# Performance work log

Measured on AMD Instinct MI355X. Metric: run time of the kernel, lower is better.

The kernel has to match this reference:

```python
import jax, jax.numpy as jnp
import numpy as np

B, T, I, H = 64, 188, 512, 1024
R = H  # recurrent_size == hidden_size (required for the cell math to be consistent)


def setup_inputs() -> dict:
    key = jax.random.key(0)
    ks = jax.random.split(key, 6)
    stdv = 1.0 / np.sqrt(H)
    u = lambda k, shape: jax.random.uniform(k, shape, jnp.float32, -stdv, stdv)
    return {
        "x": jax.random.normal(ks[0], (B, T, I), jnp.float32),
        "h0": jnp.zeros((B, R), jnp.float32),
        "c0": jnp.zeros((B, H), jnp.float32),
        "weight_ih": u(ks[1], (4 * H, I)),
        "weight_hh": u(ks[2], (4 * H, R)),
        "weight_rec": u(ks[3], (2 * R, H)),
        "bias": u(ks[4], (4 * H,)),
        "lengths": jax.random.randint(ks[5], (B,), 1, T + 1),
    }


def reference(x, h0, c0, weight_ih, weight_hh, weight_rec, bias, lengths):
    # length_matrix[j][t] == 1 iff t < lengths[j]; state is zeroed where 0
    mask = (jnp.arange(T)[:, None] < lengths[None, :]).astype(x.dtype)[:, :, None]  # [T,B,1]
    # precompute input projections for all timesteps: [T, B, 4H]
    pre_x = jnp.einsum('bti,gi->tbg', x, weight_ih) + bias

    def step(carry, inp):
        h, c = carry
        px, m = inp
        pre = px + h @ weight_hh.T           # [B, 4H]
        pre_c = c @ weight_rec.T             # [B, 2R] (peephole)
        i = jax.nn.sigmoid(pre[:, :H] + pre_c[:, :H])
        f = jax.nn.sigmoid(pre[:, H:2 * H] + pre_c[:, H:2 * H])
        g = jnp.tanh(pre[:, 2 * H:3 * H])
        c_new = f * c + i * g
        o = jax.nn.sigmoid(pre[:, 3 * H:] + c_new)
        h_new = o * jnp.tanh(c_new)
        h_new = h_new * m  # zero finished sequences (index_fill_ with 0)
        c_new = c_new * m
        return (h_new, c_new), (h_new, c_new)

    (_, _), (hs, cs) = jax.lax.scan(step, (h0, c0), (pre_x, mask))
    # stack over time then transpose(0,1) as in torch -> [B, T, H]
    return jnp.swapaxes(hs, 0, 1), jnp.swapaxes(cs, 0, 1)
```

## Files before the change

kernel.cpp:

```cpp
#include <hip/hip_runtime.h>


#define T_N 188

#define WS_PX     0UL
#define WS_XB     98566144UL
#define WS_WIHB   110886912UL
#define WS_WCOMB  115081216UL
#define WS_HST    127664128UL
#define WS_CST    127926272UL
#define WS_FLAGS  128188416UL
#define WS_WRECLO 128192512UL
#define WS_CSTLO  132386816UL

typedef __attribute__((ext_vector_type(8))) short short8;
typedef __attribute__((ext_vector_type(4))) float f4;

__device__ __forceinline__ float b2f(unsigned short u) {
    union { unsigned int i; float f; } v; v.i = ((unsigned int)u) << 16; return v.f;
}
__device__ __forceinline__ unsigned short f2b(float f) {
    unsigned int u = __float_as_uint(f);
    return (unsigned short)((u + 0x7FFFu + ((u >> 16) & 1u)) >> 16);
}
__device__ __forceinline__ float sigf(float x) { return 1.0f / (1.0f + __expf(-x)); }
__device__ __forceinline__ float tanh_(float x) {
    float e = __expf(2.0f * x); return 1.0f - 2.0f / (e + 1.0f);
}
#define MFMA(a, b, c) __builtin_amdgcn_mfma_f32_16x16x32_bf16((a), (b), (c), 0, 0, 0)

#define LD16(dst, addr) \
    asm volatile("global_load_dwordx4 %0, %1, off sc0 sc1" : "=&v"(dst) : "v"(addr))

#define BALLAST(bal)                                                       \
    _Pragma("unroll")                                                      \
    for (int u_ = 0; u_ < 16; ++u_) bal = __builtin_fmaf(bal, 1.0000001f, 1e-7f)

__device__ __forceinline__ f4 px_init(const unsigned short* px, int t, int gate, int jg, int brow) {
    unsigned long long pv =
        *(const unsigned long long*)(px + ((long)(t * 4 + gate) * 1024 + jg) * 64 + brow);
    f4 r;
    r[0] = b2f((unsigned short)pv);
    r[1] = b2f((unsigned short)(pv >> 16));
    r[2] = b2f((unsigned short)(pv >> 32));
    r[3] = b2f((unsigned short)(pv >> 48));
    return r;
}

__global__ void k_prep(const float* __restrict__ x, const float* __restrict__ h0,
                       const float* __restrict__ c0, const float* __restrict__ wih,
                       const float* __restrict__ whh, const float* __restrict__ wrec,
                       unsigned short* __restrict__ xb, unsigned short* __restrict__ wihb,
                       unsigned short* __restrict__ wcomb, unsigned short* __restrict__ hst,
                       unsigned short* __restrict__ cst, unsigned short* __restrict__ wreclo,
                       unsigned short* __restrict__ cstlo, int* __restrict__ flags) {
    const long NX4 = 1540096, NWIH4 = 524288, NWHH4 = 1048576, NWREC4 = 524288, NH4 = 16384;
    const long total = NX4 + NWIH4 + NWHH4 + NWREC4 + NH4 + NH4;
    long gtid = (long)blockIdx.x * blockDim.x + threadIdx.x;
    for (long i = gtid; i < total; i += (long)gridDim.x * blockDim.x) {
        const float* src; unsigned short* dst; unsigned short* lo_dst = nullptr; long off = i;
        if (off < NX4)                   { src = x;    dst = xb; }
        else if ((off -= NX4) < NWIH4)   { src = wih;  dst = wihb; }
        else if ((off -= NWIH4) < NWHH4) { src = whh;  dst = wcomb; }
        else if ((off -= NWHH4) < NWREC4){ src = wrec; dst = wcomb + 4194304; lo_dst = wreclo; }
        else if ((off -= NWREC4) < NH4)  { src = h0;   dst = hst + 65536; }
        else { off -= NH4;                 src = c0;   dst = cst + 65536; lo_dst = cstlo + 65536; }
        float4 v = ((const float4*)src)[off];
        unsigned short hx = f2b(v.x), hy = f2b(v.y), hz = f2b(v.z), hw = f2b(v.w);
        unsigned long long o = (unsigned long long)hx
            | ((unsigned long long)hy << 16)
            | ((unsigned long long)hz << 32)
            | ((unsigned long long)hw << 48);
        *(unsigned long long*)(dst + off * 4) = o;
        if (lo_dst) {
            unsigned long long l = (unsigned long long)f2b(v.x - b2f(hx))
                | ((unsigned long long)f2b(v.y - b2f(hy)) << 16)
                | ((unsigned long long)f2b(v.z - b2f(hz)) << 32)
                | ((unsigned long long)f2b(v.w - b2f(hw)) << 48);
            *(unsigned long long*)(lo_dst + off * 4) = l;
        }
    }
    if (gtid < 1024) flags[gtid] = 0;
}

__global__ void __launch_bounds__(256) k_px(const unsigned short* __restrict__ xb,
                                            const unsigned short* __restrict__ wihb,
                                            const float* __restrict__ bias,
                                            unsigned short* __restrict__ px) {
    const int t = blockIdx.y;
    const int wv = threadIdx.x >> 6, lane = threadIdx.x & 63;
    const int col = lane & 15, quad = lane >> 4;
    const int n = blockIdx.x * 64 + wv * 16 + col;
    const float bn = bias[n];
    f4 acc[4];
#pragma unroll
    for (int mt = 0; mt < 4; ++mt) { acc[mt][0] = bn; acc[mt][1] = bn; acc[mt][2] = bn; acc[mt][3] = bn; }
    const unsigned short* bp = wihb + n * 512 + quad * 8;
#pragma unroll 4
    for (int kk = 0; kk < 16; ++kk) {
        short8 bf = *(const short8*)(bp + kk * 32);
#pragma unroll
        for (int mt = 0; mt < 4; ++mt) {
            const unsigned short* ap = xb + ((mt * 16 + col) * 188 + t) * 512 + kk * 32 + quad * 8;
            short8 af = *(const short8*)ap;
            acc[mt] = MFMA(af, bf, acc[mt]);
        }
    }
    const long pb = ((long)(t * 4 + (n >> 10)) * 1024 + (n & 1023)) * 64;
#pragma unroll
    for (int mt = 0; mt < 4; ++mt) {
        unsigned long long o = (unsigned long long)f2b(acc[mt][0])
            | ((unsigned long long)f2b(acc[mt][1]) << 16)
            | ((unsigned long long)f2b(acc[mt][2]) << 32)
            | ((unsigned long long)f2b(acc[mt][3]) << 48);
        *(unsigned long long*)(px + pb + mt * 16 + quad * 4) = o;
    }
}

__global__ void __launch_bounds__(256, 1) k_scan(
    const unsigned short* __restrict__ wcomb, const unsigned short* __restrict__ wreclo,
    const float* __restrict__ c0, const int* __restrict__ lengths,
    const unsigned short* __restrict__ px, unsigned short* __restrict__ hst,
    unsigned short* __restrict__ cst, unsigned short* __restrict__ cstlo,
    int* __restrict__ flags, float* __restrict__ out) {
    const int cu = blockIdx.x;
    const int g = cu >> 6, cig = cu & 63;
    const int jbase = cig * 16, b0 = g * 16;
    const int tid = threadIdx.x, wv = tid >> 6, lane = tid & 63;
    const int kh = wv >> 1, ts = wv & 1;
    const int kbase = kh * 512;
    const int col = lane & 15, quad = lane >> 4;

    __shared__ float pre[2][2][6][16][16];
    __shared__ float c_loc[16][16];
    __shared__ int go_word;

    short8 wf[4][16];
#pragma unroll
    for (int tile = 0; tile < 4; ++tile) {
        const unsigned short* src;
        if (ts == 0) {
            src = wcomb + (long)(tile * 1024 + jbase + col) * 1024 + kbase + quad * 8;
        } else if (tile < 2) {
            src = wcomb + (long)((4 + tile) * 1024 + jbase + col) * 1024 + kbase + quad * 8;
        } else {
            src = wreclo + (long)((tile - 2) * 1024 + jbase + col) * 1024 + kbase + quad * 8;
        }
#pragma unroll
        for (int kk = 0; kk < 16; ++kk) wf[tile][kk] = *(const short8*)(src + kk * 32);
    }
    {
        int b = tid >> 4, j = tid & 15;
        c_loc[b][j] = c0[(b0 + b) * 1024 + jbase + j];
    }
    if (tid == 0) go_word = 0;
    const int my_len = lengths[b0 + (tid >> 4)];
    float bal = (float)lane + 1.0f;
    __syncthreads();

    float* out_h = out;
    float* out_c = out + 12320768;

    for (int t = 0; t < T_N; ++t) {
        const int sl_r = (t + 1) & 1, sl_w = t & 1, ps = t & 1;

        f4 pxv[4];
        if (ts == 0 && kh == 0) {
#pragma unroll
            for (int tile = 0; tile < 4; ++tile)
                pxv[tile] = px_init(px, t, tile, jbase + col, b0 + quad * 4);
        }

        if (t > 0) {
            if (wv == 0) {
                const int* fp = flags + g * 64 + lane;
                for (;;) {
                    int a = __hip_atomic_load(fp, __ATOMIC_RELAXED, __HIP_MEMORY_SCOPE_AGENT);
                    if (__all(a >= t)) break;
                    BALLAST(bal);
                }
                if (lane == 0)
                    __hip_atomic_store(&go_word, t, __ATOMIC_RELAXED, __HIP_MEMORY_SCOPE_WORKGROUP);
            } else {
                for (;;) {
                    int gw = __hip_atomic_load(&go_word, __ATOMIC_RELAXED, __HIP_MEMORY_SCOPE_WORKGROUP);
                    if (gw >= t) break;
                    BALLAST(bal);
                }
            }
            asm volatile("" ::: "memory");
        }

        const int sbase = sl_r * 65536 + (b0 + col) * 1024 + kbase + quad * 8;

        if (ts == 0) {
            const unsigned short* hp = hst + sbase;
            short8 hbuf[16];
#pragma unroll
            for (int kk = 0; kk < 16; ++kk) LD16(hbuf[kk], hp + kk * 32);
            f4 acc[4];
#pragma unroll
            for (int tile = 0; tile < 4; ++tile) {
                if (kh == 0) acc[tile] = pxv[tile];
                else { acc[tile][0] = 0.f; acc[tile][1] = 0.f; acc[tile][2] = 0.f; acc[tile][3] = 0.f; }
            }
            asm volatile("s_waitcnt vmcnt(0)" ::: "memory");
            __builtin_amdgcn_sched_barrier(0);
#pragma unroll
            for (int kk = 0; kk < 16; ++kk) {
                acc[0] = MFMA(hbuf[kk], wf[0][kk], acc[0]);
                acc[1] = MFMA(hbuf[kk], wf[1][kk], acc[1]);
                acc[2] = MFMA(hbuf[kk], wf[2][kk], acc[2]);
                acc[3] = MFMA(hbuf[kk], wf[3][kk], acc[3]);
            }
#pragma unroll
            for (int tile = 0; tile < 4; ++tile)
#pragma unroll
                for (int r = 0; r < 4; ++r) pre[ps][kh][tile][quad * 4 + r][col] = acc[tile][r];
        } else {
            const unsigned short* cph = cst + sbase;
            const unsigned short* cpl = cstlo + sbase;
            short8 chb[16], clb[16];
#pragma unroll
            for (int kk = 0; kk < 16; ++kk) LD16(chb[kk], cph + kk * 32);
#pragma unroll
            for (int kk = 0; kk < 16; ++kk) LD16(clb[kk], cpl + kk * 32);
            f4 a0 = {0.f, 0.f, 0.f, 0.f}, a1 = a0, a2 = a0, a3 = a0, a4 = a0, a5 = a0;
            asm volatile("s_waitcnt vmcnt(0)" ::: "memory");
            __builtin_amdgcn_sched_barrier(0);
#pragma unroll
            for (int kk = 0; kk < 16; ++kk) {
                a0 = MFMA(chb[kk], wf[0][kk], a0);
                a1 = MFMA(chb[kk], wf[1][kk], a1);
                a2 = MFMA(chb[kk], wf[2][kk], a2);
                a3 = MFMA(chb[kk], wf[3][kk], a3);
                a4 = MFMA(clb[kk], wf[0][kk], a4);
                a5 = MFMA(clb[kk], wf[1][kk], a5);
            }
#pragma unroll
            for (int r = 0; r < 4; ++r) {
                pre[ps][kh][4][quad * 4 + r][col] = a0[r] + a2[r] + a4[r];
                pre[ps][kh][5][quad * 4 + r][col] = a1[r] + a3[r] + a5[r];
            }
        }
        __syncthreads();

        float hn, cn; long ob;
        {
            const int b = tid >> 4, j = tid & 15;
            float pi = pre[ps][0][0][b][j] + pre[ps][1][0][b][j] + pre[ps][0][4][b][j] + pre[ps][1][4][b][j];
            float pf = pre[ps][0][1][b][j] + pre[ps][1][1][b][j] + pre[ps][0][5][b][j] + pre[ps][1][5][b][j];
            float pg = pre[ps][0][2][b][j] + pre[ps][1][2][b][j];
            float po = pre[ps][0][3][b][j] + pre[ps][1][3][b][j];
            const float cprev = c_loc[b][j];
            const float iv = sigf(pi), fv = sigf(pf), gv = tanh_(pg);
            cn = fv * cprev + iv * gv;
            float ov = sigf(po + cn);
            hn = ov * tanh_(cn);
            if (t >= my_len) { hn = 0.f; cn = 0.f; }
            c_loc[b][j] = cn;
            ob = (long)(b0 + b) * 192512 + (long)t * 1024 + jbase + j;
            const int sidx = sl_w * 65536 + (b0 + b) * 1024 + jbase + j;
            unsigned short hb  = f2b(hn);
            unsigned short chb2 = f2b(cn);
            unsigned short clb2 = f2b(cn - b2f(chb2));
            __hip_atomic_store(&hst[sidx],  hb,   __ATOMIC_RELAXED, __HIP_MEMORY_SCOPE_AGENT);
            __hip_atomic_store(&cst[sidx],  chb2, __ATOMIC_RELAXED, __HIP_MEMORY_SCOPE_AGENT);
            __hip_atomic_store(&cstlo[sidx], clb2, __ATOMIC_RELAXED, __HIP_MEMORY_SCOPE_AGENT);
        }
        asm volatile("s_waitcnt vmcnt(0)" ::: "memory");
        __syncthreads();
        if (tid == 0)
            __hip_atomic_store(&flags[cu], t + 1, __ATOMIC_RELAXED, __HIP_MEMORY_SCOPE_AGENT);
        out_h[ob] = hn;
        out_c[ob] = cn;
    }
    asm volatile("" :: "v"(bal));
}

extern "C" void kernel_launch(void* const* d_in, const int* in_sizes, int n_in,
                              void* d_out, int out_size, void* d_ws, size_t ws_size,
                              hipStream_t stream) {
    const float* x    = (const float*)d_in[0];
    const float* h0   = (const float*)d_in[1];
    const float* c0   = (const float*)d_in[2];
    const float* wih  = (const float*)d_in[3];
    const float* whh  = (const float*)d_in[4];
    const float* wrec = (const float*)d_in[5];
    const float* bias = (const float*)d_in[6];
    const int* lengths = (const int*)d_in[7];

    char* ws = (char*)d_ws;
    unsigned short* px     = (unsigned short*)(ws + WS_PX);
    unsigned short* xb     = (unsigned short*)(ws + WS_XB);
    unsigned short* wihb   = (unsigned short*)(ws + WS_WIHB);
    unsigned short* wcomb  = (unsigned short*)(ws + WS_WCOMB);
    unsigned short* hst    = (unsigned short*)(ws + WS_HST);
    unsigned short* cst    = (unsigned short*)(ws + WS_CST);
    unsigned short* wreclo = (unsigned short*)(ws + WS_WRECLO);
    unsigned short* cstlo  = (unsigned short*)(ws + WS_CSTLO);
    int* flags             = (int*)(ws + WS_FLAGS);
    float* out = (float*)d_out;

    hipLaunchKernelGGL(k_prep, dim3(2048), dim3(256), 0, stream,
                       x, h0, c0, wih, whh, wrec, xb, wihb, wcomb, hst, cst, wreclo, cstlo, flags);
    hipLaunchKernelGGL(k_px, dim3(64, 188), dim3(256), 0, stream, xb, wihb, bias, px);
    hipLaunchKernelGGL(k_scan, dim3(256), dim3(256), 0, stream,
                       wcomb, wreclo, c0, lengths, px, hst, cst, cstlo, flags, out);
}
```

Baseline: 1.658 ms.

## Split recurrent matmul K-dimension across all four waves and use per-wave flags

Each of the four waves now handles a quarter of the K dimension for every gate and peephole tile, replacing the earlier split of two K-halves by two tile sets. This balances MFMA work evenly across waves and shortens each wave's dependent chain. The second __syncthreads after the state stores is removed: each wave publishes its own flag, and the poller reads four flags per CU with one dwordx4 load. The spin-wait ballast is also widened to four independent FMA chains. The cost is more shared-memory partials to reduce and more flag traffic. The flag array now needs four times as many slots, and it is unclear whether the host zeroes that larger range.

```diff
diff --git a/kernel.cpp b/kernel.cpp
--- a/kernel.cpp
+++ b/kernel.cpp
@@ -15,6 +15,7 @@
 
 typedef __attribute__((ext_vector_type(8))) short short8;
 typedef __attribute__((ext_vector_type(4))) float f4;
+typedef __attribute__((ext_vector_type(4))) int int4v;
 
 __device__ __forceinline__ float b2f(unsigned short u) {
     union { unsigned int i; float f; } v; v.i = ((unsigned int)u) << 16; return v.f;
@@ -32,9 +33,14 @@
 #define LD16(dst, addr) \
     asm volatile("global_load_dwordx4 %0, %1, off sc0 sc1" : "=&v"(dst) : "v"(addr))
 
-#define BALLAST(bal)                                                       \
+#define BAL64()                                                            \
     _Pragma("unroll")                                                      \
-    for (int u_ = 0; u_ < 16; ++u_) bal = __builtin_fmaf(bal, 1.0000001f, 1e-7f)
+    for (int u_ = 0; u_ < 16; ++u_) {                                      \
+        bl0 = __builtin_fmaf(bl0, 1.0000001f, 1e-7f);                      \
+        bl1 = __builtin_fmaf(bl1, 1.0000001f, 2e-7f);                      \
+        bl2 = __builtin_fmaf(bl2, 1.0000001f, 3e-7f);                      \
+        bl3 = __builtin_fmaf(bl3, 1.0000001f, 4e-7f);                      \
+    }
 
 __device__ __forceinline__ f4 px_init(const unsigned short* px, int t, int gate, int jg, int brow) {
     unsigned long long pv =
@@ -127,35 +133,37 @@
     const int g = cu >> 6, cig = cu & 63;
     const int jbase = cig * 16, b0 = g * 16;
     const int tid = threadIdx.x, wv = tid >> 6, lane = tid & 63;
-    const int kh = wv >> 1, ts = wv & 1;
-    const int kbase = kh * 512;
+    const int kbase = wv * 256;
     const int col = lane & 15, quad = lane >> 4;
-
-    __shared__ float pre[2][2][6][16][16];
+    const int b_ = tid >> 4, j_ = tid & 15;
+
+    __shared__ float pre[2][4][6][16][16];
     __shared__ float c_loc[16][16];
     __shared__ int go_word;
 
-    short8 wf[4][16];
-#pragma unroll
-    for (int tile = 0; tile < 4; ++tile) {
-        const unsigned short* src;
-        if (ts == 0) {
-            src = wcomb + (long)(tile * 1024 + jbase + col) * 1024 + kbase + quad * 8;
-        } else if (tile < 2) {
-            src = wcomb + (long)((4 + tile) * 1024 + jbase + col) * 1024 + kbase + quad * 8;
-        } else {
-            src = wreclo + (long)((tile - 2) * 1024 + jbase + col) * 1024 + kbase + quad * 8;
-        }
-#pragma unroll
-        for (int kk = 0; kk < 16; ++kk) wf[tile][kk] = *(const short8*)(src + kk * 32);
-    }
-    {
-        int b = tid >> 4, j = tid & 15;
-        c_loc[b][j] = c0[(b0 + b) * 1024 + jbase + j];
-    }
+    short8 wg[4][8];
+    short8 wh[2][8];
+    short8 wl[2][8];
+#pragma unroll
+    for (int gate = 0; gate < 4; ++gate) {
+        const unsigned short* src = wcomb + (long)(gate * 1024 + jbase + col) * 1024 + kbase + quad * 8;
+#pragma unroll
+        for (int kk = 0; kk < 8; ++kk) wg[gate][kk] = *(const short8*)(src + kk * 32);
+    }
+#pragma unroll
+    for (int tl = 0; tl < 2; ++tl) {
+        const unsigned short* sh = wcomb + (long)((4 + tl) * 1024 + jbase + col) * 1024 + kbase + quad * 8;
+        const unsigned short* sl = wreclo + (long)(tl * 1024 + jbase + col) * 1024 + kbase + quad * 8;
+#pragma unroll
+        for (int kk = 0; kk < 8; ++kk) {
+            wh[tl][kk] = *(const short8*)(sh + kk * 32);
+            wl[tl][kk] = *(const short8*)(sl + kk * 32);
+        }
+    }
+    c_loc[b_][j_] = c0[(b0 + b_) * 1024 + jbase + j_];
     if (tid == 0) go_word = 0;
-    const int my_len = lengths[b0 + (tid >> 4)];
-    float bal = (float)lane + 1.0f;
+    const int my_len = lengths[b0 + b_];
+    float bl0 = (float)lane + 1.0f, bl1 = bl0 + 0.5f, bl2 = bl0 + 0.25f, bl3 = bl0 + 0.125f;
     __syncthreads();
 
     float* out_h = out;
@@ -165,7 +173,7 @@
         const int sl_r = (t + 1) & 1, sl_w = t & 1, ps = t & 1;
 
         f4 pxv[4];
-        if (ts == 0 && kh == 0) {
+        if (wv == 0) {
 #pragma unroll
             for (int tile = 0; tile < 4; ++tile)
                 pxv[tile] = px_init(px, t, tile, jbase + col, b0 + quad * 4);
@@ -173,11 +181,16 @@
 
         if (t > 0) {
             if (wv == 0) {
-                const int* fp = flags + g * 64 + lane;
+                const int* fp = flags + (g * 64 + lane) * 4;
                 for (;;) {
-                    int a = __hip_atomic_load(fp, __ATOMIC_RELAXED, __HIP_MEMORY_SCOPE_AGENT);
-                    if (__all(a >= t)) break;
-                    BALLAST(bal);
+                    int4v fvv;
+                    asm volatile("global_load_dwordx4 %0, %1, off sc0 sc1" : "=&v"(fvv) : "v"(fp));
+                    asm volatile("s_waitcnt vmcnt(0)" ::: "memory");
+                    int m0 = fvv[0] < fvv[1] ? fvv[0] : fvv[1];
+                    int m1 = fvv[2] < fvv[3] ? fvv[2] : fvv[3];
+                    int m = m0 < m1 ? m0 : m1;
+                    if (__all(m >= t)) break;
+                    BAL64();
                 }
                 if (lane == 0)
                     __hip_atomic_store(&go_word, t, __ATOMIC_RELAXED, __HIP_MEMORY_SCOPE_WORKGROUP);
@@ -185,7 +198,7 @@
                 for (;;) {
                     int gw = __hip_atomic_load(&go_word, __ATOMIC_RELAXED, __HIP_MEMORY_SCOPE_WORKGROUP);
                     if (gw >= t) break;
-                    BALLAST(bal);
+                    BAL64();
                 }
             }
             asm volatile("" ::: "memory");
@@ -193,89 +206,82 @@
 
         const int sbase = sl_r * 65536 + (b0 + col) * 1024 + kbase + quad * 8;
 
-        if (ts == 0) {
-            const unsigned short* hp = hst + sbase;
-            short8 hbuf[16];
-#pragma unroll
-            for (int kk = 0; kk < 16; ++kk) LD16(hbuf[kk], hp + kk * 32);
-            f4 acc[4];
-#pragma unroll
-            for (int tile = 0; tile < 4; ++tile) {
-                if (kh == 0) acc[tile] = pxv[tile];
-                else { acc[tile][0] = 0.f; acc[tile][1] = 0.f; acc[tile][2] = 0.f; acc[tile][3] = 0.f; }
+        short8 hb[8], cb[8], lb[8];
+#pragma unroll
+        for (int kk = 0; kk < 8; ++kk) LD16(hb[kk], hst + sbase + kk * 32);
+#pragma unroll
+        for (int kk = 0; kk < 8; ++kk) LD16(cb[kk], cst + sbase + kk * 32);
+#pragma unroll
+        for (int kk = 0; kk < 8; ++kk) LD16(lb[kk], cstlo + sbase + kk * 32);
+
+        f4 ag0, ag1, ag2, ag3;
+        if (wv == 0) { ag0 = pxv[0]; ag1 = pxv[1]; ag2 = pxv[2]; ag3 = pxv[3]; }
+        else {
+            ag0[0] = 0.f; ag0[1] = 0.f; ag0[2] = 0.f; ag0[3] = 0.f;
+            ag1 = ag0; ag2 = ag0; ag3 = ag0;
+        }
+        f4 ap0 = {0.f, 0.f, 0.f, 0.f}, ap1 = ap0, ap2 = ap0, ap3 = ap0, ap4 = ap0, ap5 = ap0;
+
+        asm volatile("s_waitcnt vmcnt(0)" ::: "memory");
+        __builtin_amdgcn_sched_barrier(0);
+#pragma unroll
+        for (int kk = 0; kk < 8; ++kk) {
+            ag0 = MFMA(hb[kk], wg[0][kk], ag0);
+            ag1 = MFMA(hb[kk], wg[1][kk], ag1);
+            ag2 = MFMA(hb[kk], wg[2][kk], ag2);
+            ag3 = MFMA(hb[kk], wg[3][kk], ag3);
+            ap0 = MFMA(cb[kk], wh[0][kk], ap0);
+            ap1 = MFMA(cb[kk], wh[1][kk], ap1);
+            ap2 = MFMA(cb[kk], wl[0][kk], ap2);
+            ap3 = MFMA(cb[kk], wl[1][kk], ap3);
+            ap4 = MFMA(lb[kk], wh[0][kk], ap4);
+            ap5 = MFMA(lb[kk], wh[1][kk], ap5);
+        }
+#pragma unroll
+        for (int r = 0; r < 4; ++r) {
+            pre[ps][wv][0][quad * 4 + r][col] = ag0[r];
+            pre[ps][wv][1][quad * 4 + r][col] = ag1[r];
+            pre[ps][wv][2][quad * 4 + r][col] = ag2[r];
+            pre[ps][wv][3][quad * 4 + r][col] = ag3[r];
+            pre[ps][wv][4][quad * 4 + r][col] = ap0[r] + ap2[r] + ap4[r];
+            pre[ps][wv][5][quad * 4 + r][col] = ap1[r] + ap3[r] + ap5[r];
+        }
+        __syncthreads();
+
+        float hn, cn;
+        {
+            float pi = 0.f, pf = 0.f, pg = 0.f, po = 0.f;
+#pragma unroll
+            for (int q = 0; q < 4; ++q) {
+                pi += pre[ps][q][0][b_][j_] + pre[ps][q][4][b_][j_];
+                pf += pre[ps][q][1][b_][j_] + pre[ps][q][5][b_][j_];
+                pg += pre[ps][q][2][b_][j_];
+                po += pre[ps][q][3][b_][j_];
             }
-            asm volatile("s_waitcnt vmcnt(0)" ::: "memory");
-            __builtin_amdgcn_sched_barrier(0);
-#pragma unroll
-            for (int kk = 0; kk < 16; ++kk) {
-                acc[0] = MFMA(hbuf[kk], wf[0][kk], acc[0]);
-                acc[1] = MFMA(hbuf[kk], wf[1][kk], acc[1]);
-                acc[2] = MFMA(hbuf[kk], wf[2][kk], acc[2]);
-                acc[3] = MFMA(hbuf[kk], wf[3][kk], acc[3]);
-            }
-#pragma unroll
-            for (int tile = 0; tile < 4; ++tile)
-#pragma unroll
-                for (int r = 0; r < 4; ++r) pre[ps][kh][tile][quad * 4 + r][col] = acc[tile][r];
-        } else {
-            const unsigned short* cph = cst + sbase;
-            const unsigned short* cpl = cstlo + sbase;
-            short8 chb[16], clb[16];
-#pragma unroll
-            for (int kk = 0; kk < 16; ++kk) LD16(chb[kk], cph + kk * 32);
-#pragma unroll
-            for (int kk = 0; kk < 16; ++kk) LD16(clb[kk], cpl + kk * 32);
-            f4 a0 = {0.f, 0.f, 0.f, 0.f}, a1 = a0, a2 = a0, a3 = a0, a4 = a0, a5 = a0;
-            asm volatile("s_waitcnt vmcnt(0)" ::: "memory");
-            __builtin_amdgcn_sched_barrier(0);
-#pragma unroll
-            for (int kk = 0; kk < 16; ++kk) {
-                a0 = MFMA(chb[kk], wf[0][kk], a0);
-                a1 = MFMA(chb[kk], wf[1][kk], a1);
-                a2 = MFMA(chb[kk], wf[2][kk], a2);
-                a3 = MFMA(chb[kk], wf[3][kk], a3);
-                a4 = MFMA(clb[kk], wf[0][kk], a4);
-                a5 = MFMA(clb[kk], wf[1][kk], a5);
-            }
-#pragma unroll
-            for (int r = 0; r < 4; ++r) {
-                pre[ps][kh][4][quad * 4 + r][col] = a0[r] + a2[r] + a4[r];
-                pre[ps][kh][5][quad * 4 + r][col] = a1[r] + a3[r] + a5[r];
-            }
-        }
-        __syncthreads();
-
-        float hn, cn; long ob;
-        {
-            const int b = tid >> 4, j = tid & 15;
-            float pi = pre[ps][0][0][b][j] + pre[ps][1][0][b][j] + pre[ps][0][4][b][j] + pre[ps][1][4][b][j];
-            float pf = pre[ps][0][1][b][j] + pre[ps][1][1][b][j] + pre[ps][0][5][b][j] + pre[ps][1][5][b][j];
-            float pg = pre[ps][0][2][b][j] + pre[ps][1][2][b][j];
-            float po = pre[ps][0][3][b][j] + pre[ps][1][3][b][j];
-            const float cprev = c_loc[b][j];
+            const float cprev = c_loc[b_][j_];
             const float iv = sigf(pi), fv = sigf(pf), gv = tanh_(pg);
             cn = fv * cprev + iv * gv;
             float ov = sigf(po + cn);
             hn = ov * tanh_(cn);
             if (t >= my_len) { hn = 0.f; cn = 0.f; }
-            c_loc[b][j] = cn;
-            ob = (long)(b0 + b) * 192512 + (long)t * 1024 + jbase + j;
-            const int sidx = sl_w * 65536 + (b0 + b) * 1024 + jbase + j;
-            unsigned short hb  = f2b(hn);
-            unsigned short chb2 = f2b(cn);
-            unsigned short clb2 = f2b(cn - b2f(chb2));
-            __hip_atomic_store(&hst[sidx],  hb,   __ATOMIC_RELAXED, __HIP_MEMORY_SCOPE_AGENT);
-            __hip_atomic_store(&cst[sidx],  chb2, __ATOMIC_RELAXED, __HIP_MEMORY_SCOPE_AGENT);
-            __hip_atomic_store(&cstlo[sidx], clb2, __ATOMIC_RELAXED, __HIP_MEMORY_SCOPE_AGENT);
+            c_loc[b_][j_] = cn;
+            const int sidx = sl_w * 65536 + (b0 + b_) * 1024 + jbase + j_;
+            unsigned short hbw  = f2b(hn);
+            unsigned short chw  = f2b(cn);
+            unsigned short clw  = f2b(cn - b2f(chw));
+            __hip_atomic_store(&hst[sidx],   hbw, __ATOMIC_RELAXED, __HIP_MEMORY_SCOPE_AGENT);
+            __hip_atomic_store(&cst[sidx],   chw, __ATOMIC_RELAXED, __HIP_MEMORY_SCOPE_AGENT);
+            __hip_atomic_store(&cstlo[sidx], clw, __ATOMIC_RELAXED, __HIP_MEMORY_SCOPE_AGENT);
         }
         asm volatile("s_waitcnt vmcnt(0)" ::: "memory");
-        __syncthreads();
-        if (tid == 0)
-            __hip_atomic_store(&flags[cu], t + 1, __ATOMIC_RELAXED, __HIP_MEMORY_SCOPE_AGENT);
+        if (lane == 0)
+            __hip_atomic_store(&flags[cu * 4 + wv], t + 1,
+                               __ATOMIC_RELAXED, __HIP_MEMORY_SCOPE_AGENT);
+        const long ob = (long)(b0 + b_) * 192512 + (long)t * 1024 + jbase + j_;
         out_h[ob] = hn;
         out_c[ob] = cn;
     }
-    asm volatile("" :: "v"(bal));
+    asm volatile("" :: "v"(bl0), "v"(bl1), "v"(bl2), "v"(bl3));
 }
 
 extern "C" void kernel_launch(void* const* d_in, const int* in_sizes, int n_in,
```

Result: slower. 1.691 ms (+2.0%).

## Convert recurrent weights to bf16 in scan kernel; widen input-projection tiles

Applied to the files above, without the earlier changes.

The scan kernel now loads the fp32 whh and wrec matrices directly and converts them to bf16 (with a hi/lo split for wrec) into registers at startup. This drops the prep kernel's conversion pass and its workspace round trip. Separately, the input-projection GEMM kernel gives each wave a 4x4 grid of MFMA tiles instead of 4x1, reusing A and B fragments more and launching a quarter as many blocks. The cost is twice as much global read in scan's prologue, more conversion work there, and higher register pressure in k_px.

```diff
diff --git a/kernel.cpp b/kernel.cpp
--- a/kernel.cpp
+++ b/kernel.cpp
@@ -49,22 +49,18 @@
 
 __global__ void k_prep(const float* __restrict__ x, const float* __restrict__ h0,
                        const float* __restrict__ c0, const float* __restrict__ wih,
-                       const float* __restrict__ whh, const float* __restrict__ wrec,
                        unsigned short* __restrict__ xb, unsigned short* __restrict__ wihb,
-                       unsigned short* __restrict__ wcomb, unsigned short* __restrict__ hst,
-                       unsigned short* __restrict__ cst, unsigned short* __restrict__ wreclo,
+                       unsigned short* __restrict__ hst, unsigned short* __restrict__ cst,
                        unsigned short* __restrict__ cstlo, int* __restrict__ flags) {
-    const long NX4 = 1540096, NWIH4 = 524288, NWHH4 = 1048576, NWREC4 = 524288, NH4 = 16384;
-    const long total = NX4 + NWIH4 + NWHH4 + NWREC4 + NH4 + NH4;
+    const long NX4 = 1540096, NWIH4 = 524288, NH4 = 16384;
+    const long total = NX4 + NWIH4 + NH4 + NH4;
     long gtid = (long)blockIdx.x * blockDim.x + threadIdx.x;
     for (long i = gtid; i < total; i += (long)gridDim.x * blockDim.x) {
         const float* src; unsigned short* dst; unsigned short* lo_dst = nullptr; long off = i;
-        if (off < NX4)                   { src = x;    dst = xb; }
-        else if ((off -= NX4) < NWIH4)   { src = wih;  dst = wihb; }
-        else if ((off -= NWIH4) < NWHH4) { src = whh;  dst = wcomb; }
-        else if ((off -= NWHH4) < NWREC4){ src = wrec; dst = wcomb + 4194304; lo_dst = wreclo; }
-        else if ((off -= NWREC4) < NH4)  { src = h0;   dst = hst + 65536; }
-        else { off -= NH4;                 src = c0;   dst = cst + 65536; lo_dst = cstlo + 65536; }
+        if (off < NX4)                  { src = x;   dst = xb; }
+        else if ((off -= NX4) < NWIH4)  { src = wih; dst = wihb; }
+        else if ((off -= NWIH4) < NH4)  { src = h0;  dst = hst + 65536; }
+        else { off -= NH4;                src = c0;  dst = cst + 65536; lo_dst = cstlo + 65536; }
         float4 v = ((const float4*)src)[off];
         unsigned short hx = f2b(v.x), hy = f2b(v.y), hz = f2b(v.z), hw = f2b(v.w);
         unsigned long long o = (unsigned long long)hx
@@ -90,35 +86,48 @@
     const int t = blockIdx.y;
     const int wv = threadIdx.x >> 6, lane = threadIdx.x & 63;
     const int col = lane & 15, quad = lane >> 4;
-    const int n = blockIdx.x * 64 + wv * 16 + col;
-    const float bn = bias[n];
-    f4 acc[4];
-#pragma unroll
-    for (int mt = 0; mt < 4; ++mt) { acc[mt][0] = bn; acc[mt][1] = bn; acc[mt][2] = bn; acc[mt][3] = bn; }
-    const unsigned short* bp = wihb + n * 512 + quad * 8;
+    const int nb = blockIdx.x * 256 + wv * 64;
+    f4 acc[4][4];
+#pragma unroll
+    for (int nt = 0; nt < 4; ++nt) {
+        const float bn = bias[nb + nt * 16 + col];
+#pragma unroll
+        for (int mt = 0; mt < 4; ++mt) {
+            acc[mt][nt][0] = bn; acc[mt][nt][1] = bn; acc[mt][nt][2] = bn; acc[mt][nt][3] = bn;
+        }
+    }
 #pragma unroll 4
     for (int kk = 0; kk < 16; ++kk) {
-        short8 bf = *(const short8*)(bp + kk * 32);
+        short8 bf[4], af[4];
+#pragma unroll
+        for (int nt = 0; nt < 4; ++nt)
+            bf[nt] = *(const short8*)(wihb + (nb + nt * 16 + col) * 512 + kk * 32 + quad * 8);
+#pragma unroll
+        for (int mt = 0; mt < 4; ++mt)
+            af[mt] = *(const short8*)(xb + ((mt * 16 + col) * 188 + t) * 512 + kk * 32 + quad * 8);
+#pragma unroll
+        for (int mt = 0; mt < 4; ++mt)
+#pragma unroll
+            for (int nt = 0; nt < 4; ++nt)
+                acc[mt][nt] = MFMA(af[mt], bf[nt], acc[mt][nt]);
+    }
+#pragma unroll
+    for (int nt = 0; nt < 4; ++nt) {
+        const int n = nb + nt * 16 + col;
+        const long pb = ((long)(t * 4 + (n >> 10)) * 1024 + (n & 1023)) * 64;
 #pragma unroll
         for (int mt = 0; mt < 4; ++mt) {
-            const unsigned short* ap = xb + ((mt * 16 + col) * 188 + t) * 512 + kk * 32 + quad * 8;
-            short8 af = *(const short8*)ap;
-            acc[mt] = MFMA(af, bf, acc[mt]);
-        }
-    }
-    const long pb = ((long)(t * 4 + (n >> 10)) * 1024 + (n & 1023)) * 64;
-#pragma unroll
-    for (int mt = 0; mt < 4; ++mt) {
-        unsigned long long o = (unsigned long long)f2b(acc[mt][0])
-            | ((unsigned long long)f2b(acc[mt][1]) << 16)
-            | ((unsigned long long)f2b(acc[mt][2]) << 32)
-            | ((unsigned long long)f2b(acc[mt][3]) << 48);
-        *(unsigned long long*)(px + pb + mt * 16 + quad * 4) = o;
+            unsigned long long o = (unsigned long long)f2b(acc[mt][nt][0])
+                | ((unsigned long long)f2b(acc[mt][nt][1]) << 16)
+                | ((unsigned long long)f2b(acc[mt][nt][2]) << 32)
+                | ((unsigned long long)f2b(acc[mt][nt][3]) << 48);
+            *(unsigned long long*)(px + pb + mt * 16 + quad * 4) = o;
+        }
     }
 }
 
 __global__ void __launch_bounds__(256, 1) k_scan(
-    const unsigned short* __restrict__ wcomb, const unsigned short* __restrict__ wreclo,
+    const float* __restrict__ whh, const float* __restrict__ wrec,
     const float* __restrict__ c0, const int* __restrict__ lengths,
     const unsigned short* __restrict__ px, unsigned short* __restrict__ hst,
     unsigned short* __restrict__ cst, unsigned short* __restrict__ cstlo,
@@ -136,18 +145,40 @@
     __shared__ int go_word;
 
     short8 wf[4][16];
-#pragma unroll
-    for (int tile = 0; tile < 4; ++tile) {
-        const unsigned short* src;
-        if (ts == 0) {
-            src = wcomb + (long)(tile * 1024 + jbase + col) * 1024 + kbase + quad * 8;
-        } else if (tile < 2) {
-            src = wcomb + (long)((4 + tile) * 1024 + jbase + col) * 1024 + kbase + quad * 8;
-        } else {
-            src = wreclo + (long)((tile - 2) * 1024 + jbase + col) * 1024 + kbase + quad * 8;
-        }
-#pragma unroll
-        for (int kk = 0; kk < 16; ++kk) wf[tile][kk] = *(const short8*)(src + kk * 32);
+    if (ts == 0) {
+#pragma unroll
+        for (int tile = 0; tile < 4; ++tile) {
+            const float* src = whh + (long)(tile * 1024 + jbase + col) * 1024 + kbase + quad * 8;
+#pragma unroll
+            for (int kk = 0; kk < 16; ++kk) {
+                float4 a = *(const float4*)(src + kk * 32);
+                float4 b = *(const float4*)(src + kk * 32 + 4);
+                union { unsigned short u[8]; short8 s; } P;
+                P.u[0] = f2b(a.x); P.u[1] = f2b(a.y); P.u[2] = f2b(a.z); P.u[3] = f2b(a.w);
+                P.u[4] = f2b(b.x); P.u[5] = f2b(b.y); P.u[6] = f2b(b.z); P.u[7] = f2b(b.w);
+                wf[tile][kk] = P.s;
+            }
+        }
+    } else {
+#pragma unroll
+        for (int tl = 0; tl < 2; ++tl) {
+            const float* src = wrec + (long)(tl * 1024 + jbase + col) * 1024 + kbase + quad * 8;
+#pragma unroll
+            for (int kk = 0; kk < 16; ++kk) {
+                float4 a = *(const float4*)(src + kk * 32);
+                float4 b = *(const float4*)(src + kk * 32 + 4);
+                float w[8] = {a.x, a.y, a.z, a.w, b.x, b.y, b.z, b.w};
+                union { unsigned short u[8]; short8 s; } H, L;
+#pragma unroll
+                for (int e = 0; e < 8; ++e) {
+                    unsigned short hi = f2b(w[e]);
+                    H.u[e] = hi;
+                    L.u[e] = f2b(w[e] - b2f(hi));
+                }
+                wf[tl][kk] = H.s;
+                wf[2 + tl][kk] = L.s;
+            }
+        }
     }
     {
         int b = tid >> 4, j = tid & 15;
@@ -294,17 +325,15 @@
     unsigned short* px     = (unsigned short*)(ws + WS_PX);
     unsigned short* xb     = (unsigned short*)(ws + WS_XB);
     unsigned short* wihb   = (unsigned short*)(ws + WS_WIHB);
-    unsigned short* wcomb  = (unsigned short*)(ws + WS_WCOMB);
     unsigned short* hst    = (unsigned short*)(ws + WS_HST);
     unsigned short* cst    = (unsigned short*)(ws + WS_CST);
-    unsigned short* wreclo = (unsigned short*)(ws + WS_WRECLO);
     unsigned short* cstlo  = (unsigned short*)(ws + WS_CSTLO);
     int* flags             = (int*)(ws + WS_FLAGS);
     float* out = (float*)d_out;
 
     hipLaunchKernelGGL(k_prep, dim3(2048), dim3(256), 0, stream,
-                       x, h0, c0, wih, whh, wrec, xb, wihb, wcomb, hst, cst, wreclo, cstlo, flags);
-    hipLaunchKernelGGL(k_px, dim3(64, 188), dim3(256), 0, stream, xb, wihb, bias, px);
+                       x, h0, c0, wih, xb, wihb, hst, cst, cstlo, flags);
+    hipLaunchKernelGGL(k_px, dim3(16, 188), dim3(256), 0, stream, xb, wihb, bias, px);
     hipLaunchKernelGGL(k_scan, dim3(256), dim3(256), 0, stream,
-                       wcomb, wreclo, c0, lengths, px, hst, cst, cstlo, flags, out);
-}
+                       whh, wrec, c0, lengths, px, hst, cst, cstlo, flags, out);
+}
```

Measured after the change: 1.446 ms. 12.8% less time.
